# Optimization experiments

Measured on AMD Instinct MI355X. Metric: run time of the kernel, lower is better.

The kernel has to match this reference:

```python
import jax, jax.numpy as jnp
import numpy as np

N_HEADS = 32
D_IN = 128 + 256 + 1024  # 1408
D_HID = 256
D_OUT = 3


def setup_inputs() -> dict:
    key = jax.random.key(0)
    k1, k2, k3, k4, k5 = jax.random.split(key, 5)
    B = 16384
    total_feat = jax.random.normal(k1, (B, D_IN), dtype=jnp.float32)
    # Stacked per-head parameters. Original zero-inits the second Linear;
    # we use small random values so the baseline exercises non-trivial math.
    s1 = 1.0 / np.sqrt(D_IN)
    s2 = 1.0 / np.sqrt(D_HID)
    W1 = jax.random.uniform(k2, (N_HEADS, D_IN, D_HID), jnp.float32, -s1, s1)
    b1 = jax.random.uniform(k3, (N_HEADS, D_HID), jnp.float32, -s1, s1)
    W2 = jax.random.uniform(k4, (N_HEADS, D_HID, D_OUT), jnp.float32, -s2, s2)
    b2 = jax.random.uniform(k5, (N_HEADS, D_OUT), jnp.float32, -s2, s2)
    return {"total_feat": total_feat, "W1": W1, "b1": b1, "W2": W2, "b2": b2}


def reference(total_feat, W1, b1, W2, b2):
    # 32 heads of Linear(1408->256) -> ReLU -> Linear(256->3), batched.
    h = jax.nn.relu(jnp.einsum('bf,hfo->bho', total_feat, W1) + b1)  # [B,32,256]
    out = jnp.einsum('bho,hop->bhp', h, W2) + b2                     # [B,32,3]
    B = total_feat.shape[0]
    # concat(dim=-1) over heads == reshape since each head emits 3 contiguous values
    return out.reshape(B, N_HEADS * D_OUT)                           # [B,96]
```

## Files before the change

kernel.cpp:

```cpp
#include <hip/hip_runtime.h>
#include <hip/hip_bf16.h>
#include <stdint.h>

#define D_IN    1408
#define D_HID   256
#define N_HEADS 32
#define BATCH   16384

#define BM 256
#define BN 256
#define BK 64
#define KTILES (D_IN / BK)
#define NSEG 8

typedef unsigned short u16;
typedef short short8 __attribute__((ext_vector_type(8)));
typedef float f32x4 __attribute__((ext_vector_type(4)));

__device__ __forceinline__ u16 f2b(float f) {
  __hip_bfloat16 h = __float2bfloat16(f);
  return *(u16*)&h;
}

__device__ __forceinline__ void gload_lds16(const void* g, void* l) {
  __builtin_amdgcn_global_load_lds(
      (const __attribute__((address_space(1))) uint32_t*)((const uint32_t*)g),
      (__attribute__((address_space(3))) uint32_t*)((uint32_t*)l),
      16, 0, 0);
}

__global__ void convert_x(const float4* __restrict__ X, ushort4* __restrict__ Xb) {
  int i = blockIdx.x * blockDim.x + threadIdx.x;
  float4 v = X[i];
  ushort4 o;
  o.x = f2b(v.x); o.y = f2b(v.y); o.z = f2b(v.z); o.w = f2b(v.w);
  Xb[i] = o;
}

__global__ void transpose_w1(const float* __restrict__ W1, u16* __restrict__ W1T) {
  __shared__ u16 tile[64][68];
  const int h = blockIdx.z;
  const int f0 = blockIdx.x * 64;
  const int o0 = blockIdx.y * 64;
  const int tx = threadIdx.x;
  const int ty = threadIdx.y;
  const size_t ib = (size_t)h * D_IN * D_HID;
  #pragma unroll
  for (int i = ty; i < 64; i += 4)
    tile[i][tx] = f2b(W1[ib + (size_t)(f0 + i) * D_HID + o0 + tx]);
  __syncthreads();
  const size_t ob = (size_t)h * D_HID * D_IN;
  #pragma unroll
  for (int pass = 0; pass < 4; ++pass) {
    int r = pass * 16 + ty * 4 + (tx >> 4);
    int c = (tx & 15) * 4;
    ushort4 v;
    v.x = tile[c + 0][r]; v.y = tile[c + 1][r];
    v.z = tile[c + 2][r]; v.w = tile[c + 3][r];
    *(ushort4*)&W1T[ob + (size_t)(o0 + r) * D_IN + f0 + c] = v;
  }
}

__global__ __launch_bounds__(512, 2) void mano_gemm(
    const u16* __restrict__ X,
    const u16* __restrict__ W1T,
    const float* __restrict__ b1,
    const float* __restrict__ W2,
    const float* __restrict__ b2,
    float* __restrict__ out)
{
  __shared__ __align__(16) u16 As[2][BM * BK];
  __shared__ __align__(16) u16 Bs[2][BN * BK];
  __shared__ __align__(16) float scr[3072];
  __shared__ float b1L[256];
  __shared__ float w2L[768];
  __shared__ float b2L[3];

  const int tid  = threadIdx.x;
  const int lane = tid & 63;
  const int wid  = tid >> 6;
  const int quad = lane >> 4;
  const int l15  = lane & 15;
  const int wm   = wid >> 2;
  const int wn   = wid & 3;

  const int bid  = blockIdx.x;
  const int head = (bid & 7) * 4 + ((bid >> 3) & 3);
  const int u2   = bid >> 5;

  const u16* Bu = W1T + (size_t)head * D_HID * D_IN;

  if (tid < 256) b1L[tid] = b1[head * D_HID + tid];
  for (int i = tid; i < 768; i += 512) w2L[i] = W2[(size_t)head * D_HID * 3 + i];
  if (tid < 3)  b2L[tid] = b2[head * 3 + tid];

  int off[2][2];
  #pragma unroll
  for (int c = 0; c < 2; ++c) {
    int ci = c * 512 + tid;
    int rl = ci >> 3;
    int k8 = (ci & 7) ^ (rl & 7);
    #pragma unroll
    for (int h = 0; h < 2; ++h)
      off[h][c] = (h * 128 + rl) * D_IN + k8 * 8;
  }

#define STG_A(BI, H, P) do { _Pragma("unroll")                                 \
    for (int c = 0; c < 2; ++c)                                                \
      gload_lds16((P) + off[H][c],                                             \
                  &As[BI][((H) * 1024 + c * 512 + wid * 64) * 8]); } while (0)
#define STG_B(BI, H, P) do { _Pragma("unroll")                                 \
    for (int c = 0; c < 2; ++c)                                                \
      gload_lds16((P) + off[H][c],                                             \
                  &Bs[BI][((H) * 1024 + c * 512 + wid * 64) * 8]); } while (0)

  const int wm16l = wm * 16 + l15;
  const int wn16l = wn * 16 + l15;
  const int rx  = l15 & 7;
  const int co0 = (quad ^ rx) * 16;
  const int co1 = ((4 + quad) ^ rx) * 16;

#define LDAF(BI, mf, ks)                                                       \
  (*(const short8*)((const char*)&As[BI][0] +                                  \
                    ((mf) * 32 + wm16l) * 128 + ((ks) ? co1 : co0)))
#define LDBF(BI, nf, ks)                                                       \
  (*(const short8*)((const char*)&Bs[BI][0] +                                  \
                    (nf) * 8192 + wn16l * 128 + ((ks) ? co1 : co0)))
#define MM(mi, nj, ks)                                                         \
  acc[mi][nj] = __builtin_amdgcn_mfma_f32_16x16x32_bf16(                       \
      a[(mi) & 3][ks], b[nj][ks], acc[mi][nj], 0, 0, 0)

  f32x4 acc[8][4];
  #pragma unroll
  for (int i = 0; i < 8; ++i)
    #pragma unroll
    for (int j = 0; j < 4; ++j)
      acc[i][j] = f32x4{0.f, 0.f, 0.f, 0.f};

  short8 a[4][2], b[4][2];

#define DO_TILE(BI, B0P, B0SK, A0P, A0SK, B1P, B1SK, A1P, A1SK, DRAIN)         \
  do {                                                                         \
              \
    _Pragma("unroll") for (int mf = 0; mf < 4; ++mf) {                         \
      a[mf][0] = LDAF(BI, mf, 0); a[mf][1] = LDAF(BI, mf, 1); }                \
    _Pragma("unroll") for (int nf = 0; nf < 2; ++nf) {                         \
      b[nf][0] = LDBF(BI, nf, 0); b[nf][1] = LDBF(BI, nf, 1); }                \
    if (!(B0SK)) STG_B((BI) ^ 1, 0, B0P);                                      \
    __builtin_amdgcn_s_setprio(1);                                             \
    _Pragma("unroll") for (int mf = 0; mf < 4; ++mf) {                         \
      MM(mf, 0, 0); MM(mf, 0, 1); MM(mf, 1, 0); MM(mf, 1, 1); }                \
    __builtin_amdgcn_s_setprio(0);                                             \
    __builtin_amdgcn_s_barrier();                                              \
         \
    _Pragma("unroll") for (int nf = 2; nf < 4; ++nf) {                         \
      b[nf][0] = LDBF(BI, nf, 0); b[nf][1] = LDBF(BI, nf, 1); }                \
    if (!(A0SK)) STG_A(BI, 0, A0P);                                            \
    __builtin_amdgcn_s_setprio(1);                                             \
    _Pragma("unroll") for (int mf = 0; mf < 4; ++mf) {                         \
      MM(mf, 2, 0); MM(mf, 2, 1); MM(mf, 3, 0); MM(mf, 3, 1); }                \
    __builtin_amdgcn_s_setprio(0);                                             \
    __builtin_amdgcn_s_barrier();                                              \
         \
    _Pragma("unroll") for (int i = 0; i < 4; ++i) {                            \
      a[i][0] = LDAF(BI, 4 + i, 0); a[i][1] = LDAF(BI, 4 + i, 1); }            \
    if (!(B1SK)) STG_B(BI, 1, B1P);                                            \
    __builtin_amdgcn_s_setprio(1);                                             \
    _Pragma("unroll") for (int i = 0; i < 4; ++i) {                            \
      MM(4 + i, 2, 0); MM(4 + i, 2, 1); MM(4 + i, 3, 0); MM(4 + i, 3, 1); }    \
    __builtin_amdgcn_s_setprio(0);                                             \
    __builtin_amdgcn_s_barrier();                                              \
                     \
    if (!(A1SK)) STG_A(BI, 1, A1P);                                            \
    __builtin_amdgcn_s_setprio(1);                                             \
    _Pragma("unroll") for (int i = 0; i < 4; ++i) {                            \
      MM(4 + i, 0, 0); MM(4 + i, 0, 1); MM(4 + i, 1, 0); MM(4 + i, 1, 1); }    \
    __builtin_amdgcn_s_setprio(0);                                             \
    if (DRAIN) { asm volatile("s_waitcnt vmcnt(0)" ::: "memory"); }            \
    else       { asm volatile("s_waitcnt vmcnt(6)" ::: "memory"); }            \
    __builtin_amdgcn_s_barrier();                                              \
  } while (0)

  {
    const u16* Au0 = X + (size_t)(u2 * 256) * D_IN;
    STG_A(0, 0, Au0);
    STG_B(0, 1, Bu);
    STG_A(0, 1, Au0);
    STG_B(0, 0, Bu);
    STG_A(1, 0, Au0 + BK);
    STG_B(1, 1, Bu + BK);
    STG_A(1, 1, Au0 + BK);
    asm volatile("s_waitcnt lgkmcnt(0)" ::: "memory");
    asm volatile("s_waitcnt vmcnt(6)" ::: "memory");
    __builtin_amdgcn_s_barrier();
  }

  #pragma unroll 1
  for (int g = 0; g < NSEG; ++g) {
    const u16* AuC = X + (size_t)((g * 8 + u2) * 256) * D_IN;
    const u16* AuN = AuC + (size_t)(8 * 256) * D_IN;
    const bool lastseg = (g == NSEG - 1);

    #pragma unroll 1
    for (int j = 0; j < KTILES / 2; ++j) {
      const int kt0 = 2 * j;
      const int kp1 = kt0 + 1;
      const int kp2 = kt0 + 2;
      const int kp3 = kt0 + 3;
      const bool w2f = (kp2 >= KTILES), w3f = (kp3 >= KTILES);
      const int k2m = w2f ? kp2 - KTILES : kp2;
      const int k3m = w3f ? kp3 - KTILES : kp3;
      const u16* Bp1 = Bu + kp1 * BK;
      const u16* Bp2 = Bu + k2m * BK;
      const u16* Bp3 = Bu + k3m * BK;
      const u16* Ap2 = (w2f ? AuN : AuC) + k2m * BK;
      const u16* Ap3 = (w3f ? AuN : AuC) + k3m * BK;
      const bool sk2 = lastseg && w2f;
      const bool sk3 = lastseg && w3f;
      const bool drain = lastseg && (j == KTILES / 2 - 1);

      DO_TILE(0, Bp1, false, Ap2, sk2, Bp2, sk2, Ap2, sk2, drain);
      DO_TILE(1, Bp2, sk2,   Ap3, sk3, Bp3, sk3, Ap3, sk3, drain);
    }

    {
      float b1v[4], w2v[4][3];
      #pragma unroll
      for (int nf = 0; nf < 4; ++nf) {
        int col = nf * 64 + wn16l;
        b1v[nf] = b1L[col];
        #pragma unroll
        for (int p = 0; p < 3; ++p) w2v[nf][p] = w2L[col * 3 + p];
      }
      const int m0 = (g * 8 + u2) * 256;

      #pragma unroll
      for (int mf = 0; mf < 8; ++mf) {
        float ps[4][3];
        #pragma unroll
        for (int r = 0; r < 4; ++r)
          #pragma unroll
          for (int p = 0; p < 3; ++p) ps[r][p] = 0.f;

        #pragma unroll
        for (int nf = 0; nf < 4; ++nf)
          #pragma unroll
          for (int r = 0; r < 4; ++r) {
            float h = acc[mf][nf][r] + b1v[nf];
            h = h > 0.f ? h : 0.f;
            #pragma unroll
            for (int p = 0; p < 3; ++p)
              ps[r][p] = fmaf(h, w2v[nf][p], ps[r][p]);
          }

        #pragma unroll
        for (int mask = 1; mask < 16; mask <<= 1)
          #pragma unroll
          for (int r = 0; r < 4; ++r)
            #pragma unroll
            for (int p = 0; p < 3; ++p)
              ps[r][p] += __shfl_xor(ps[r][p], mask, 64);

        if (l15 == 0) {
          int row = mf * 32 + wm * 16 + quad * 4;
          #pragma unroll
          for (int r = 0; r < 4; ++r)
            #pragma unroll
            for (int p = 0; p < 3; ++p)
              scr[((row + r) * 3 + p) * 4 + wn] = ps[r][p];
        }
      }
      asm volatile("s_waitcnt lgkmcnt(0)" ::: "memory");
      __builtin_amdgcn_s_barrier();

      for (int i = tid; i < BM * 3; i += 512) {
        int row = i / 3, p = i - row * 3;
        float v = scr[i * 4 + 0] + scr[i * 4 + 1] + scr[i * 4 + 2]
                + scr[i * 4 + 3] + b2L[p];
        out[(size_t)(m0 + row) * (N_HEADS * 3) + head * 3 + p] = v;
      }

      #pragma unroll
      for (int i = 0; i < 8; ++i)
        #pragma unroll
        for (int jj = 0; jj < 4; ++jj)
          acc[i][jj] = f32x4{0.f, 0.f, 0.f, 0.f};
    }
  }

#undef STG_A
#undef STG_B
#undef LDAF
#undef LDBF
#undef MM
#undef DO_TILE
}

extern "C" void kernel_launch(void* const* d_in, const int* in_sizes, int n_in,
                              void* d_out, int out_size, void* d_ws, size_t ws_size,
                              hipStream_t stream) {
  const float* X  = (const float*)d_in[0];
  const float* W1 = (const float*)d_in[1];
  const float* b1 = (const float*)d_in[2];
  const float* W2 = (const float*)d_in[3];
  const float* b2 = (const float*)d_in[4];

  u16* Xb  = (u16*)d_ws;
  u16* W1T = (u16*)((char*)d_ws + (size_t)BATCH * D_IN * 2);

  convert_x<<<(BATCH * D_IN / 4) / 256, 256, 0, stream>>>(
      (const float4*)X, (ushort4*)Xb);

  transpose_w1<<<dim3(D_IN / 64, D_HID / 64, N_HEADS), dim3(64, 4), 0, stream>>>(W1, W1T);

  mano_gemm<<<dim3(256), 512, 0, stream>>>(
      Xb, W1T, b1, W2, b2, (float*)d_out);
}
```

Measured before the change: 544.4 us.

## Shrink GEMM tiles to 128x256x32, double grid, and fuse prep kernels

Halves the M tile and K step of the fused per-head MLP GEMM, doubling the grid to 512 blocks and raising the occupancy target to 4 blocks per CU. The four-phase software pipeline is replaced with a simple double-buffered loop that waits on all loads each tile. The X conversion and W1 transpose are merged into one launch to save launch overhead. The intent is better CU occupancy and load balance, at the cost of less data reuse per tile, more barriers and a shallower prefetch.

```diff
diff --git a/kernel.cpp b/kernel.cpp
--- a/kernel.cpp
+++ b/kernel.cpp
@@ -7,9 +7,9 @@
 #define N_HEADS 32
 #define BATCH   16384
 
-#define BM 256
+#define BM 128
 #define BN 256
-#define BK 64
+#define BK 32
 #define KTILES (D_IN / BK)
 #define NSEG 8
 
@@ -29,21 +29,26 @@
       16, 0, 0);
 }
 
-__global__ void convert_x(const float4* __restrict__ X, ushort4* __restrict__ Xb) {
-  int i = blockIdx.x * blockDim.x + threadIdx.x;
-  float4 v = X[i];
-  ushort4 o;
-  o.x = f2b(v.x); o.y = f2b(v.y); o.z = f2b(v.z); o.w = f2b(v.w);
-  Xb[i] = o;
-}
-
-__global__ void transpose_w1(const float* __restrict__ W1, u16* __restrict__ W1T) {
+#define CONV_BLOCKS 22528
+__global__ void prep(const float4* __restrict__ X, ushort4* __restrict__ Xb,
+                     const float* __restrict__ W1, u16* __restrict__ W1T) {
+  const int bid = blockIdx.x;
+  const int tid = threadIdx.x;
+  if (bid < CONV_BLOCKS) {
+    int i = bid * 256 + tid;
+    float4 v = X[i];
+    ushort4 o;
+    o.x = f2b(v.x); o.y = f2b(v.y); o.z = f2b(v.z); o.w = f2b(v.w);
+    Xb[i] = o;
+    return;
+  }
   __shared__ u16 tile[64][68];
-  const int h = blockIdx.z;
-  const int f0 = blockIdx.x * 64;
-  const int o0 = blockIdx.y * 64;
-  const int tx = threadIdx.x;
-  const int ty = threadIdx.y;
+  const int b  = bid - CONV_BLOCKS;
+  const int f0 = (b % 22) * 64;
+  const int o0 = ((b / 22) & 3) * 64;
+  const int h  = b / 88;
+  const int tx = tid & 63;
+  const int ty = tid >> 6;
   const size_t ib = (size_t)h * D_IN * D_HID;
   #pragma unroll
   for (int i = ty; i < 64; i += 4)
@@ -61,7 +66,7 @@
   }
 }
 
-__global__ __launch_bounds__(512, 2) void mano_gemm(
+__global__ __launch_bounds__(512, 4) void mano_gemm(
     const u16* __restrict__ X,
     const u16* __restrict__ W1T,
     const float* __restrict__ b1,
@@ -71,7 +76,7 @@
 {
   __shared__ __align__(16) u16 As[2][BM * BK];
   __shared__ __align__(16) u16 Bs[2][BN * BK];
-  __shared__ __align__(16) float scr[3072];
+  __shared__ __align__(16) float scr[1536];
   __shared__ float b1L[256];
   __shared__ float w2L[768];
   __shared__ float b2L[3];
@@ -86,7 +91,7 @@
 
   const int bid  = blockIdx.x;
   const int head = (bid & 7) * 4 + ((bid >> 3) & 3);
-  const int u2   = bid >> 5;
+  const int u    = bid >> 5;
 
   const u16* Bu = W1T + (size_t)head * D_HID * D_IN;
 
@@ -94,148 +99,98 @@
   for (int i = tid; i < 768; i += 512) w2L[i] = W2[(size_t)head * D_HID * 3 + i];
   if (tid < 3)  b2L[tid] = b2[head * 3 + tid];
 
-  int off[2][2];
-  #pragma unroll
-  for (int c = 0; c < 2; ++c) {
-    int ci = c * 512 + tid;
-    int rl = ci >> 3;
-    int k8 = (ci & 7) ^ (rl & 7);
-    #pragma unroll
-    for (int h = 0; h < 2; ++h)
-      off[h][c] = (h * 128 + rl) * D_IN + k8 * 8;
-  }
-
-#define STG_A(BI, H, P) do { _Pragma("unroll")                                 \
-    for (int c = 0; c < 2; ++c)                                                \
-      gload_lds16((P) + off[H][c],                                             \
-                  &As[BI][((H) * 1024 + c * 512 + wid * 64) * 8]); } while (0)
-#define STG_B(BI, H, P) do { _Pragma("unroll")                                 \
-    for (int c = 0; c < 2; ++c)                                                \
-      gload_lds16((P) + off[H][c],                                             \
-                  &Bs[BI][((H) * 1024 + c * 512 + wid * 64) * 8]); } while (0)
-
-  const int wm16l = wm * 16 + l15;
-  const int wn16l = wn * 16 + l15;
-  const int rx  = l15 & 7;
-  const int co0 = (quad ^ rx) * 16;
-  const int co1 = ((4 + quad) ^ rx) * 16;
-
-#define LDAF(BI, mf, ks)                                                       \
-  (*(const short8*)((const char*)&As[BI][0] +                                  \
-                    ((mf) * 32 + wm16l) * 128 + ((ks) ? co1 : co0)))
-#define LDBF(BI, nf, ks)                                                       \
-  (*(const short8*)((const char*)&Bs[BI][0] +                                  \
-                    (nf) * 8192 + wn16l * 128 + ((ks) ? co1 : co0)))
-#define MM(mi, nj, ks)                                                         \
-  acc[mi][nj] = __builtin_amdgcn_mfma_f32_16x16x32_bf16(                       \
-      a[(mi) & 3][ks], b[nj][ks], acc[mi][nj], 0, 0, 0)
-
-  f32x4 acc[8][4];
-  #pragma unroll
-  for (int i = 0; i < 8; ++i)
+  int aoff;
+  {
+    int row = tid >> 2, c = tid & 3;
+    aoff = row * D_IN + (c ^ ((row >> 1) & 3)) * 8;
+  }
+  int boff[2];
+  #pragma unroll
+  for (int cc = 0; cc < 2; ++cc) {
+    int ci = cc * 512 + tid;
+    int row = ci >> 2, c = ci & 3;
+    boff[cc] = row * D_IN + (c ^ ((row >> 1) & 3)) * 8;
+  }
+
+  const int p16 = (quad ^ ((l15 >> 1) & 3)) * 16;
+  const int abase = (wm * 64 + l15) * 64 + p16;
+  const int bbase = (wn * 64 + l15) * 64 + p16;
+
+#define STG(BI, AP, BP) do {                                                   \
+    gload_lds16((AP) + aoff, &As[BI][wid * 512]);                              \
+    _Pragma("unroll")                                                          \
+    for (int cc = 0; cc < 2; ++cc)                                             \
+      gload_lds16((BP) + boff[cc], &Bs[BI][(cc * 512 + wid * 64) * 8]);        \
+  } while (0)
+
+  f32x4 acc[4][4];
+  #pragma unroll
+  for (int i = 0; i < 4; ++i)
     #pragma unroll
     for (int j = 0; j < 4; ++j)
       acc[i][j] = f32x4{0.f, 0.f, 0.f, 0.f};
 
-  short8 a[4][2], b[4][2];
-
-#define DO_TILE(BI, B0P, B0SK, A0P, A0SK, B1P, B1SK, A1P, A1SK, DRAIN)         \
-  do {                                                                         \
-              \
-    _Pragma("unroll") for (int mf = 0; mf < 4; ++mf) {                         \
-      a[mf][0] = LDAF(BI, mf, 0); a[mf][1] = LDAF(BI, mf, 1); }                \
-    _Pragma("unroll") for (int nf = 0; nf < 2; ++nf) {                         \
-      b[nf][0] = LDBF(BI, nf, 0); b[nf][1] = LDBF(BI, nf, 1); }                \
-    if (!(B0SK)) STG_B((BI) ^ 1, 0, B0P);                                      \
+  short8 a[4], b[4];
+
+#define TILE(BI, AP, BP, SK) do {                                              \
+    if (!(SK)) STG((BI) ^ 1, AP, BP);                                          \
+    _Pragma("unroll") for (int mf = 0; mf < 4; ++mf)                           \
+      a[mf] = *(const short8*)((const char*)&As[BI][0] + abase + mf * 1024);   \
+    _Pragma("unroll") for (int nf = 0; nf < 4; ++nf)                           \
+      b[nf] = *(const short8*)((const char*)&Bs[BI][0] + bbase + nf * 1024);   \
     __builtin_amdgcn_s_setprio(1);                                             \
-    _Pragma("unroll") for (int mf = 0; mf < 4; ++mf) {                         \
-      MM(mf, 0, 0); MM(mf, 0, 1); MM(mf, 1, 0); MM(mf, 1, 1); }                \
+    _Pragma("unroll") for (int mf = 0; mf < 4; ++mf)                           \
+      _Pragma("unroll") for (int nf = 0; nf < 4; ++nf)                         \
+        acc[mf][nf] = __builtin_amdgcn_mfma_f32_16x16x32_bf16(                 \
+            a[mf], b[nf], acc[mf][nf], 0, 0, 0);                               \
     __builtin_amdgcn_s_setprio(0);                                             \
-    __builtin_amdgcn_s_barrier();                                              \
-         \
-    _Pragma("unroll") for (int nf = 2; nf < 4; ++nf) {                         \
-      b[nf][0] = LDBF(BI, nf, 0); b[nf][1] = LDBF(BI, nf, 1); }                \
-    if (!(A0SK)) STG_A(BI, 0, A0P);                                            \
-    __builtin_amdgcn_s_setprio(1);                                             \
-    _Pragma("unroll") for (int mf = 0; mf < 4; ++mf) {                         \
-      MM(mf, 2, 0); MM(mf, 2, 1); MM(mf, 3, 0); MM(mf, 3, 1); }                \
-    __builtin_amdgcn_s_setprio(0);                                             \
-    __builtin_amdgcn_s_barrier();                                              \
-         \
-    _Pragma("unroll") for (int i = 0; i < 4; ++i) {                            \
-      a[i][0] = LDAF(BI, 4 + i, 0); a[i][1] = LDAF(BI, 4 + i, 1); }            \
-    if (!(B1SK)) STG_B(BI, 1, B1P);                                            \
-    __builtin_amdgcn_s_setprio(1);                                             \
-    _Pragma("unroll") for (int i = 0; i < 4; ++i) {                            \
-      MM(4 + i, 2, 0); MM(4 + i, 2, 1); MM(4 + i, 3, 0); MM(4 + i, 3, 1); }    \
-    __builtin_amdgcn_s_setprio(0);                                             \
-    __builtin_amdgcn_s_barrier();                                              \
-                     \
-    if (!(A1SK)) STG_A(BI, 1, A1P);                                            \
-    __builtin_amdgcn_s_setprio(1);                                             \
-    _Pragma("unroll") for (int i = 0; i < 4; ++i) {                            \
-      MM(4 + i, 0, 0); MM(4 + i, 0, 1); MM(4 + i, 1, 0); MM(4 + i, 1, 1); }    \
-    __builtin_amdgcn_s_setprio(0);                                             \
-    if (DRAIN) { asm volatile("s_waitcnt vmcnt(0)" ::: "memory"); }            \
-    else       { asm volatile("s_waitcnt vmcnt(6)" ::: "memory"); }            \
+    asm volatile("s_waitcnt vmcnt(0)" ::: "memory");                           \
     __builtin_amdgcn_s_barrier();                                              \
   } while (0)
 
   {
-    const u16* Au0 = X + (size_t)(u2 * 256) * D_IN;
-    STG_A(0, 0, Au0);
-    STG_B(0, 1, Bu);
-    STG_A(0, 1, Au0);
-    STG_B(0, 0, Bu);
-    STG_A(1, 0, Au0 + BK);
-    STG_B(1, 1, Bu + BK);
-    STG_A(1, 1, Au0 + BK);
+    const u16* A0 = X + (size_t)(u * BM) * D_IN;
+    STG(0, A0, Bu);
     asm volatile("s_waitcnt lgkmcnt(0)" ::: "memory");
-    asm volatile("s_waitcnt vmcnt(6)" ::: "memory");
+    asm volatile("s_waitcnt vmcnt(0)" ::: "memory");
     __builtin_amdgcn_s_barrier();
   }
 
   #pragma unroll 1
   for (int g = 0; g < NSEG; ++g) {
-    const u16* AuC = X + (size_t)((g * 8 + u2) * 256) * D_IN;
-    const u16* AuN = AuC + (size_t)(8 * 256) * D_IN;
+    const u16* AuC = X + (size_t)((g * 16 + u) * BM) * D_IN;
+    const u16* AuN = AuC + (size_t)(16 * BM) * D_IN;
     const bool lastseg = (g == NSEG - 1);
 
     #pragma unroll 1
     for (int j = 0; j < KTILES / 2; ++j) {
-      const int kt0 = 2 * j;
-      const int kp1 = kt0 + 1;
-      const int kp2 = kt0 + 2;
-      const int kp3 = kt0 + 3;
-      const bool w2f = (kp2 >= KTILES), w3f = (kp3 >= KTILES);
-      const int k2m = w2f ? kp2 - KTILES : kp2;
-      const int k3m = w3f ? kp3 - KTILES : kp3;
-      const u16* Bp1 = Bu + kp1 * BK;
+      const int kt1 = 2 * j + 1;
+      const int kt2 = 2 * j + 2;
+      const bool wrap = (kt2 >= KTILES);
+      const int k2m  = wrap ? 0 : kt2;
+      const u16* Ap1 = AuC + kt1 * BK;
+      const u16* Bp1 = Bu + kt1 * BK;
+      const u16* Ap2 = (wrap ? AuN : AuC) + k2m * BK;
       const u16* Bp2 = Bu + k2m * BK;
-      const u16* Bp3 = Bu + k3m * BK;
-      const u16* Ap2 = (w2f ? AuN : AuC) + k2m * BK;
-      const u16* Ap3 = (w3f ? AuN : AuC) + k3m * BK;
-      const bool sk2 = lastseg && w2f;
-      const bool sk3 = lastseg && w3f;
-      const bool drain = lastseg && (j == KTILES / 2 - 1);
-
-      DO_TILE(0, Bp1, false, Ap2, sk2, Bp2, sk2, Ap2, sk2, drain);
-      DO_TILE(1, Bp2, sk2,   Ap3, sk3, Bp3, sk3, Ap3, sk3, drain);
+      const bool sk2 = lastseg && wrap;
+
+      TILE(0, Ap1, Bp1, false);
+      TILE(1, Ap2, Bp2, sk2);
     }
 
     {
       float b1v[4], w2v[4][3];
       #pragma unroll
       for (int nf = 0; nf < 4; ++nf) {
-        int col = nf * 64 + wn16l;
+        int col = wn * 64 + nf * 16 + l15;
         b1v[nf] = b1L[col];
         #pragma unroll
         for (int p = 0; p < 3; ++p) w2v[nf][p] = w2L[col * 3 + p];
       }
-      const int m0 = (g * 8 + u2) * 256;
+      const int m0 = (g * 16 + u) * BM;
 
       #pragma unroll
-      for (int mf = 0; mf < 8; ++mf) {
+      for (int mf = 0; mf < 4; ++mf) {
         float ps[4][3];
         #pragma unroll
         for (int r = 0; r < 4; ++r)
@@ -262,7 +217,7 @@
               ps[r][p] += __shfl_xor(ps[r][p], mask, 64);
 
         if (l15 == 0) {
-          int row = mf * 32 + wm * 16 + quad * 4;
+          int row = wm * 64 + mf * 16 + quad * 4;
           #pragma unroll
           for (int r = 0; r < 4; ++r)
             #pragma unroll
@@ -281,19 +236,15 @@
       }
 
       #pragma unroll
-      for (int i = 0; i < 8; ++i)
+      for (int i = 0; i < 4; ++i)
         #pragma unroll
         for (int jj = 0; jj < 4; ++jj)
           acc[i][jj] = f32x4{0.f, 0.f, 0.f, 0.f};
     }
   }
 
-#undef STG_A
-#undef STG_B
-#undef LDAF
-#undef LDBF
-#undef MM
-#undef DO_TILE
+#undef STG
+#undef TILE
 }
 
 extern "C" void kernel_launch(void* const* d_in, const int* in_sizes, int n_in,
@@ -308,11 +259,9 @@
   u16* Xb  = (u16*)d_ws;
   u16* W1T = (u16*)((char*)d_ws + (size_t)BATCH * D_IN * 2);
 
-  convert_x<<<(BATCH * D_IN / 4) / 256, 256, 0, stream>>>(
-      (const float4*)X, (ushort4*)Xb);
-
-  transpose_w1<<<dim3(D_IN / 64, D_HID / 64, N_HEADS), dim3(64, 4), 0, stream>>>(W1, W1T);
-
-  mano_gemm<<<dim3(256), 512, 0, stream>>>(
+  prep<<<CONV_BLOCKS + (D_IN / 64) * (D_HID / 64) * N_HEADS, 256, 0, stream>>>(
+      (const float4*)X, (ushort4*)Xb, W1, W1T);
+
+  mano_gemm<<<dim3(512), 512, 0, stream>>>(
       Xb, W1T, b1, W2, b2, (float*)d_out);
 }
```

New measurement: 574.3 us. 1.06x slower.
